# Optimization experiments

Hardware: AMD Instinct MI355X
Metric: run time of the kernel (lower is better)

Reference implementation:

```python
import jax, jax.numpy as jnp
import numpy as np

TEMPERATURE = 0.5
_EPS = 1e-12  # F.normalize eps


def setup_inputs() -> dict:
    key = jax.random.key(0)
    k1, k2 = jax.random.split(key)
    N, D = 4096, 256
    z_i = jax.random.normal(k1, (N, D), dtype=jnp.float32)
    z_j = jax.random.normal(k2, (N, D), dtype=jnp.float32)
    return {"z_i": z_i, "z_j": z_j}


def _l2_normalize(x):
    # matches F.normalize(dim=-1): x / max(||x||, eps)
    norm = jnp.sqrt(jnp.sum(x * x, axis=-1, keepdims=True))
    return x / jnp.maximum(norm, _EPS)


def reference(z_i, z_j):
    n = z_i.shape[0]
    zi = _l2_normalize(z_i)
    zj = _l2_normalize(z_j)
    reps = jnp.concatenate([zi, zj], axis=0)  # [2N, D], unit rows
    # cosine similarity of unit vectors == dot product -> GEMM instead of
    # the O(N^2 * D) broadcast intermediate in the torch source
    sim = jnp.matmul(reps, reps.T) / TEMPERATURE  # [2N, 2N]
    # mask diagonal (self-similarity) with -inf
    two_n = 2 * n
    diag = jnp.eye(two_n, dtype=bool)
    sim = jnp.where(diag, -jnp.inf, sim)
    # labels: positive pair for row k is (k+N) mod 2N
    labels = jnp.concatenate([jnp.arange(n, two_n), jnp.arange(n)], axis=0)
    # cross-entropy with mean reduction
    logp = jax.nn.log_softmax(sim, axis=-1)  # -inf entries contribute 0 prob
    nll = -jnp.take_along_axis(logp, labels[:, None], axis=1)[:, 0]
    return jnp.mean(nll)
```

## Files before the change

### kernel.cpp

```cpp
#include <hip/hip_runtime.h>
#include <hip/hip_bf16.h>
#include <stdint.h>

#define N_ROWS 4096
#define D_DIM  256
#define TWO_N  8192
#define C_EXP  2.8853900817779268f

typedef __attribute__((ext_vector_type(4))) float f32x4;
typedef __attribute__((ext_vector_type(8))) int   int8v;


__global__ __launch_bounds__(256) void kprep(const float* __restrict__ zi,
                                             const float* __restrict__ zj,
                                             char* __restrict__ packed,
                                             float* __restrict__ pos,
                                             float* __restrict__ selfexp,
                                             float* __restrict__ rowsum) {
    int wave = threadIdx.x >> 6, lane = threadIdx.x & 63;
    int k = blockIdx.x * 4 + wave;
    float4 a = *(const float4*)(zi + (size_t)k * D_DIM + lane * 4);
    float4 b = *(const float4*)(zj + (size_t)k * D_DIM + lane * 4);
    float dii = a.x * a.x + a.y * a.y + a.z * a.z + a.w * a.w;
    float djj = b.x * b.x + b.y * b.y + b.z * b.z + b.w * b.w;
    float dij = a.x * b.x + a.y * b.y + a.z * b.z + a.w * b.w;
#pragma unroll
    for (int m = 1; m < 64; m <<= 1) {
        dii += __shfl_xor(dii, m, 64);
        djj += __shfl_xor(djj, m, 64);
        dij += __shfl_xor(dij, m, 64);
    }
    float si = 1.0f / fmaxf(sqrtf(dii), 1e-12f);
    float sj = 1.0f / fmaxf(sqrtf(djj), 1e-12f);

    unsigned pa = __builtin_amdgcn_cvt_pk_fp8_f32(a.x * si, a.y * si, 0, 0);
    pa = __builtin_amdgcn_cvt_pk_fp8_f32(a.z * si, a.w * si, pa, 1);
    unsigned pb = __builtin_amdgcn_cvt_pk_fp8_f32(b.x * sj, b.y * sj, 0, 0);
    pb = __builtin_amdgcn_cvt_pk_fp8_f32(b.z * sj, b.w * sj, pb, 1);

    const int f = lane >> 5, g = (lane >> 3) & 3, j = (lane & 7) * 4;
    {
        int r = k;
        int byte = ((r >> 4) * 2 + f) * 2048 + g * 512 + (r & 15) * 32 + j;
        *(unsigned*)(packed + byte) = pa;
    }
    {
        int r = k + N_ROWS;
        int byte = ((r >> 4) * 2 + f) * 2048 + g * 512 + (r & 15) * 32 + j;
        *(unsigned*)(packed + byte) = pb;
    }

    float fa0 = __builtin_amdgcn_cvt_f32_fp8(pa, 0), fa1 = __builtin_amdgcn_cvt_f32_fp8(pa, 1);
    float fa2 = __builtin_amdgcn_cvt_f32_fp8(pa, 2), fa3 = __builtin_amdgcn_cvt_f32_fp8(pa, 3);
    float fb0 = __builtin_amdgcn_cvt_f32_fp8(pb, 0), fb1 = __builtin_amdgcn_cvt_f32_fp8(pb, 1);
    float fb2 = __builtin_amdgcn_cvt_f32_fp8(pb, 2), fb3 = __builtin_amdgcn_cvt_f32_fp8(pb, 3);
    float sa = fa0 * fa0 + fa1 * fa1 + fa2 * fa2 + fa3 * fa3;
    float sb = fb0 * fb0 + fb1 * fb1 + fb2 * fb2 + fb3 * fb3;
#pragma unroll
    for (int m = 1; m < 64; m <<= 1) {
        sa += __shfl_xor(sa, m, 64);
        sb += __shfl_xor(sb, m, 64);
    }
    if (lane == 0) {
        float p = dij * si * sj * 2.0f;
        pos[k] = p;
        pos[k + N_ROWS] = p;
        selfexp[k] = __builtin_amdgcn_exp2f(sa * C_EXP);
        selfexp[k + N_ROWS] = __builtin_amdgcn_exp2f(sb * C_EXP);
    }
    if (threadIdx.x < 8) rowsum[blockIdx.x * 8 + threadIdx.x] = 0.0f;
}

__global__ __launch_bounds__(256) void kmain(const char* __restrict__ packed,
                                             float* __restrict__ rowsum) {
    __shared__ float colpart[4][256];

    const int tid = threadIdx.x;
    const int wave = tid >> 6, lane = tid & 63;
    const int l15 = lane & 15, lhi = lane >> 4;

    int b = (blockIdx.x & 7) * 132 + (blockIdx.x >> 3);
    int rt, s0, nt;
    if (b < 1024) { rt = b >> 4; s0 = (b & 15) * 2; nt = 2; }
    else          { rt = b - 1024; s0 = 32; nt = 1; }

    const int rowbaseW = rt * 128 + wave * 32;

#pragma unroll
    for (int i = 0; i < 4; ++i) colpart[wave][i * 64 + lane] = 0.0f;

    const int rtile = rt * 8 + wave * 2;
    int8v afrag[2][2];
#pragma unroll
    for (int rf = 0; rf < 2; ++rf)
#pragma unroll
        for (int f = 0; f < 2; ++f)
            afrag[rf][f] = *(const int8v*)(packed + (size_t)((rtile + rf) * 2 + f) * 2048 + lane * 32);

    float rsum[2][4];
#pragma unroll
    for (int rf = 0; rf < 2; ++rf)
#pragma unroll
        for (int r = 0; r < 4; ++r) rsum[rf][r] = 0.0f;

    for (int ti = 0; ti < nt; ++ti) {
        const int ct = (rt + s0 + ti) & 63;

#pragma unroll
        for (int sub = 0; sub < 2; ++sub) {
            const int ctile = ct * 8 + sub * 4;

            f32x4 acc[2][4];
#pragma unroll
            for (int rf = 0; rf < 2; ++rf)
#pragma unroll
                for (int cf = 0; cf < 4; ++cf) acc[rf][cf] = (f32x4){0.f, 0.f, 0.f, 0.f};

#pragma unroll
            for (int f = 0; f < 2; ++f) {
                int8v bfr[4];
#pragma unroll
                for (int cf = 0; cf < 4; ++cf)
                    bfr[cf] = *(const int8v*)(packed + (size_t)((ctile + cf) * 2 + f) * 2048 + lane * 32);
#pragma unroll
                for (int rf = 0; rf < 2; ++rf)
#pragma unroll
                    for (int cf = 0; cf < 4; ++cf)
                        acc[rf][cf] = __builtin_amdgcn_mfma_scale_f32_16x16x128_f8f6f4(
                            afrag[rf][f], bfr[cf], acc[rf][cf],
                            0, 0,
                            0, 0x7F7F7F7F,
                            0, 0x7F7F7F7F);
            }

#pragma unroll
            for (int cf = 0; cf < 4; ++cf) {
                float cacc = 0.0f;
#pragma unroll
                for (int rf = 0; rf < 2; ++rf) {
                    f32x4 cv = acc[rf][cf];
#pragma unroll
                    for (int r = 0; r < 4; ++r) {
                        float e = __builtin_amdgcn_exp2f(cv[r] * C_EXP);
                        rsum[rf][r] += e;
                        cacc += e;
                    }
                }
                cacc += __shfl_xor(cacc, 16, 64);
                cacc += __shfl_xor(cacc, 32, 64);
                if (lane < 16)
                    colpart[wave][ti * 128 + sub * 64 + cf * 16 + lane] += cacc;
            }
        }
    }

    __syncthreads();
    {
        int ti = tid >> 7;
        int c  = tid & 127;
        int s  = s0 + ti;
        if (ti < nt && s > 0) {
            int ct = (rt + s) & 63;
            atomicAdd(&rowsum[ct * 128 + c],
                      colpart[0][tid] + colpart[1][tid] +
                      colpart[2][tid] + colpart[3][tid]);
        }
    }

#pragma unroll
    for (int rf = 0; rf < 2; ++rf)
#pragma unroll
        for (int r = 0; r < 4; ++r) {
            float v = rsum[rf][r];
            v += __shfl_xor(v, 1, 64);
            v += __shfl_xor(v, 2, 64);
            v += __shfl_xor(v, 4, 64);
            v += __shfl_xor(v, 8, 64);
            if (l15 == 0)
                atomicAdd(&rowsum[rowbaseW + rf * 16 + lhi * 4 + r], v);
        }
}

__global__ __launch_bounds__(1024) void kfinal(const float* __restrict__ rowsum,
                                               const float* __restrict__ pos,
                                               const float* __restrict__ selfexp,
                                               float* __restrict__ out) {
    __shared__ float red[16];
    float local = 0.0f;
    for (int r = threadIdx.x; r < TWO_N; r += 1024)
        local += __builtin_amdgcn_logf(rowsum[r] - selfexp[r]) * 0.6931471805599453f - pos[r];
#pragma unroll
    for (int m = 1; m < 64; m <<= 1) local += __shfl_xor(local, m, 64);
    if ((threadIdx.x & 63) == 0) red[threadIdx.x >> 6] = local;
    __syncthreads();
    if (threadIdx.x == 0) {
        float t = 0.0f;
#pragma unroll
        for (int i = 0; i < 16; ++i) t += red[i];
        out[0] = t * (1.0f / (float)TWO_N);
    }
}

extern "C" void kernel_launch(void* const* d_in, const int* in_sizes, int n_in,
                              void* d_out, int out_size, void* d_ws, size_t ws_size,
                              hipStream_t stream) {
    const float* zi = (const float*)d_in[0];
    const float* zj = (const float*)d_in[1];
    float* out = (float*)d_out;

    char* packed = (char*)d_ws;
    float* rowsum = (float*)((char*)d_ws + (size_t)TWO_N * D_DIM * 2);
    float* pos = rowsum + TWO_N;
    float* selfexp = pos + TWO_N;

    kprep<<<1024, 256, 0, stream>>>(zi, zj, packed, pos, selfexp, rowsum);
    kmain<<<1056, 256, 0, stream>>>(packed, rowsum);
    kfinal<<<1, 1024, 0, stream>>>(rowsum, pos, selfexp, out);
}
```

Before: 32.01 us.

## Quantize normalized rows to FP4 and spread final reduction across blocks

Normalized embeddings are now quantized to FP4 (e2m1) with a fixed 16x prescale instead of FP8. The packed layout is halved and the MFMA scaled-matrix instruction runs in FP4 mode with a compensating exponent scale. This cuts the bytes loaded per tile and uses the faster FP4 MFMA rate, at a large cost in similarity precision that may push the loss outside tolerance. The final reduction also moves from one block to 32 blocks combined with an atomic add, and the output is zeroed in the prep kernel.

After: 27.82 us (median of 2 runs). 13.1% less time.

```diff
diff --git a/kernel.cpp b/kernel.cpp
--- a/kernel.cpp
+++ b/kernel.cpp
@@ -8,15 +8,29 @@
 #define C_EXP  2.8853900817779268f
 
 typedef __attribute__((ext_vector_type(4))) float f32x4;
+typedef __attribute__((ext_vector_type(4))) int   int4v;
 typedef __attribute__((ext_vector_type(8))) int   int8v;
 
+
+__device__ __forceinline__ float q4(float c, unsigned& code) {
+    float x = c * 16.0f;
+    unsigned s = __float_as_uint(x) >> 31;
+    float ax = fminf(fabsf(x), 6.0f);
+    unsigned q; float v;
+    if (ax < 2.0f)      { float r = rintf(ax * 2.0f); q = (unsigned)r;      v = r * 0.5f; }
+    else if (ax < 4.0f) { float r = rintf(ax);        q = (unsigned)r + 2u; v = r;        }
+    else                { float r = rintf(ax * 0.5f); q = (unsigned)r + 4u; v = r * 2.0f; }
+    code = q | (s << 3);
+    return s ? -v : v;
+}
 
 __global__ __launch_bounds__(256) void kprep(const float* __restrict__ zi,
                                              const float* __restrict__ zj,
                                              char* __restrict__ packed,
                                              float* __restrict__ pos,
                                              float* __restrict__ selfexp,
-                                             float* __restrict__ rowsum) {
+                                             float* __restrict__ rowsum,
+                                             float* __restrict__ out) {
     int wave = threadIdx.x >> 6, lane = threadIdx.x & 63;
     int k = blockIdx.x * 4 + wave;
     float4 a = *(const float4*)(zi + (size_t)k * D_DIM + lane * 4);
@@ -33,29 +47,30 @@
     float si = 1.0f / fmaxf(sqrtf(dii), 1e-12f);
     float sj = 1.0f / fmaxf(sqrtf(djj), 1e-12f);
 
-    unsigned pa = __builtin_amdgcn_cvt_pk_fp8_f32(a.x * si, a.y * si, 0, 0);
-    pa = __builtin_amdgcn_cvt_pk_fp8_f32(a.z * si, a.w * si, pa, 1);
-    unsigned pb = __builtin_amdgcn_cvt_pk_fp8_f32(b.x * sj, b.y * sj, 0, 0);
-    pb = __builtin_amdgcn_cvt_pk_fp8_f32(b.z * sj, b.w * sj, pb, 1);
-
-    const int f = lane >> 5, g = (lane >> 3) & 3, j = (lane & 7) * 4;
+    unsigned c0, c1, c2, c3;
+    float va0 = q4(a.x * si, c0), va1 = q4(a.y * si, c1);
+    float va2 = q4(a.z * si, c2), va3 = q4(a.w * si, c3);
+    unsigned na = c0 | (c1 << 4) | (c2 << 8) | (c3 << 12);
+    float vb0 = q4(b.x * sj, c0), vb1 = q4(b.y * sj, c1);
+    float vb2 = q4(b.z * sj, c2), vb3 = q4(b.w * sj, c3);
+    unsigned nb = c0 | (c1 << 4) | (c2 << 8) | (c3 << 12);
+
+    const int f = lane >> 5;
+    const int g = (lane >> 3) & 3;
+    const int off2 = 2 * (lane & 7);
     {
         int r = k;
-        int byte = ((r >> 4) * 2 + f) * 2048 + g * 512 + (r & 15) * 32 + j;
-        *(unsigned*)(packed + byte) = pa;
+        int byte = ((r >> 4) * 2 + f) * 1024 + (g * 16 + (r & 15)) * 16 + off2;
+        *(unsigned short*)(packed + byte) = (unsigned short)na;
     }
     {
         int r = k + N_ROWS;
-        int byte = ((r >> 4) * 2 + f) * 2048 + g * 512 + (r & 15) * 32 + j;
-        *(unsigned*)(packed + byte) = pb;
-    }
-
-    float fa0 = __builtin_amdgcn_cvt_f32_fp8(pa, 0), fa1 = __builtin_amdgcn_cvt_f32_fp8(pa, 1);
-    float fa2 = __builtin_amdgcn_cvt_f32_fp8(pa, 2), fa3 = __builtin_amdgcn_cvt_f32_fp8(pa, 3);
-    float fb0 = __builtin_amdgcn_cvt_f32_fp8(pb, 0), fb1 = __builtin_amdgcn_cvt_f32_fp8(pb, 1);
-    float fb2 = __builtin_amdgcn_cvt_f32_fp8(pb, 2), fb3 = __builtin_amdgcn_cvt_f32_fp8(pb, 3);
-    float sa = fa0 * fa0 + fa1 * fa1 + fa2 * fa2 + fa3 * fa3;
-    float sb = fb0 * fb0 + fb1 * fb1 + fb2 * fb2 + fb3 * fb3;
+        int byte = ((r >> 4) * 2 + f) * 1024 + (g * 16 + (r & 15)) * 16 + off2;
+        *(unsigned short*)(packed + byte) = (unsigned short)nb;
+    }
+
+    float sa = va0 * va0 + va1 * va1 + va2 * va2 + va3 * va3;
+    float sb = vb0 * vb0 + vb1 * vb1 + vb2 * vb2 + vb3 * vb3;
 #pragma unroll
     for (int m = 1; m < 64; m <<= 1) {
         sa += __shfl_xor(sa, m, 64);
@@ -65,10 +80,11 @@
         float p = dij * si * sj * 2.0f;
         pos[k] = p;
         pos[k + N_ROWS] = p;
-        selfexp[k] = __builtin_amdgcn_exp2f(sa * C_EXP);
-        selfexp[k + N_ROWS] = __builtin_amdgcn_exp2f(sb * C_EXP);
+        selfexp[k] = __builtin_amdgcn_exp2f(sa * (C_EXP / 256.0f));
+        selfexp[k + N_ROWS] = __builtin_amdgcn_exp2f(sb * (C_EXP / 256.0f));
     }
     if (threadIdx.x < 8) rowsum[blockIdx.x * 8 + threadIdx.x] = 0.0f;
+    if (blockIdx.x == 0 && threadIdx.x == 0) out[0] = 0.0f;
 }
 
 __global__ __launch_bounds__(256) void kmain(const char* __restrict__ packed,
@@ -90,12 +106,12 @@
     for (int i = 0; i < 4; ++i) colpart[wave][i * 64 + lane] = 0.0f;
 
     const int rtile = rt * 8 + wave * 2;
-    int8v afrag[2][2];
+    int4v afrag[2][2];
 #pragma unroll
     for (int rf = 0; rf < 2; ++rf)
 #pragma unroll
         for (int f = 0; f < 2; ++f)
-            afrag[rf][f] = *(const int8v*)(packed + (size_t)((rtile + rf) * 2 + f) * 2048 + lane * 32);
+            afrag[rf][f] = *(const int4v*)(packed + (size_t)((rtile + rf) * 2 + f) * 1024 + lane * 16);
 
     float rsum[2][4];
 #pragma unroll
@@ -118,19 +134,23 @@
 
 #pragma unroll
             for (int f = 0; f < 2; ++f) {
-                int8v bfr[4];
+                int4v bfr[4];
 #pragma unroll
                 for (int cf = 0; cf < 4; ++cf)
-                    bfr[cf] = *(const int8v*)(packed + (size_t)((ctile + cf) * 2 + f) * 2048 + lane * 32);
-#pragma unroll
-                for (int rf = 0; rf < 2; ++rf)
-#pragma unroll
-                    for (int cf = 0; cf < 4; ++cf)
+                    bfr[cf] = *(const int4v*)(packed + (size_t)((ctile + cf) * 2 + f) * 1024 + lane * 16);
+#pragma unroll
+                for (int rf = 0; rf < 2; ++rf) {
+                    int8v A8 = {afrag[rf][f][0], afrag[rf][f][1], afrag[rf][f][2], afrag[rf][f][3], 0, 0, 0, 0};
+#pragma unroll
+                    for (int cf = 0; cf < 4; ++cf) {
+                        int8v B8 = {bfr[cf][0], bfr[cf][1], bfr[cf][2], bfr[cf][3], 0, 0, 0, 0};
                         acc[rf][cf] = __builtin_amdgcn_mfma_scale_f32_16x16x128_f8f6f4(
-                            afrag[rf][f], bfr[cf], acc[rf][cf],
-                            0, 0,
-                            0, 0x7F7F7F7F,
-                            0, 0x7F7F7F7F);
+                            A8, B8, acc[rf][cf],
+                            4, 4,
+                            0, 0x7B7B7B7B,
+                            0, 0x7B7B7B7B);
+                    }
+                }
             }
 
 #pragma unroll
@@ -181,24 +201,19 @@
         }
 }
 
-__global__ __launch_bounds__(1024) void kfinal(const float* __restrict__ rowsum,
-                                               const float* __restrict__ pos,
-                                               const float* __restrict__ selfexp,
-                                               float* __restrict__ out) {
-    __shared__ float red[16];
-    float local = 0.0f;
-    for (int r = threadIdx.x; r < TWO_N; r += 1024)
-        local += __builtin_amdgcn_logf(rowsum[r] - selfexp[r]) * 0.6931471805599453f - pos[r];
+__global__ __launch_bounds__(256) void kfinal(const float* __restrict__ rowsum,
+                                              const float* __restrict__ pos,
+                                              const float* __restrict__ selfexp,
+                                              float* __restrict__ out) {
+    __shared__ float red[4];
+    int r = blockIdx.x * 256 + threadIdx.x;
+    float local = __builtin_amdgcn_logf(rowsum[r] - selfexp[r]) * 0.6931471805599453f - pos[r];
 #pragma unroll
     for (int m = 1; m < 64; m <<= 1) local += __shfl_xor(local, m, 64);
     if ((threadIdx.x & 63) == 0) red[threadIdx.x >> 6] = local;
     __syncthreads();
-    if (threadIdx.x == 0) {
-        float t = 0.0f;
-#pragma unroll
-        for (int i = 0; i < 16; ++i) t += red[i];
-        out[0] = t * (1.0f / (float)TWO_N);
-    }
+    if (threadIdx.x == 0)
+        atomicAdd(out, (red[0] + red[1] + red[2] + red[3]) * (1.0f / (float)TWO_N));
 }
 
 extern "C" void kernel_launch(void* const* d_in, const int* in_sizes, int n_in,
@@ -213,7 +228,7 @@
     float* pos = rowsum + TWO_N;
     float* selfexp = pos + TWO_N;
 
-    kprep<<<1024, 256, 0, stream>>>(zi, zj, packed, pos, selfexp, rowsum);
+    kprep<<<1024, 256, 0, stream>>>(zi, zj, packed, pos, selfexp, rowsum, out);
     kmain<<<1056, 256, 0, stream>>>(packed, rowsum);
-    kfinal<<<1, 1024, 0, stream>>>(rowsum, pos, selfexp, out);
-}
+    kfinal<<<32, 256, 0, stream>>>(rowsum, pos, selfexp, out);
+}
```
